# Performance work log

Measured on AMD Instinct MI355X. Metric: run time of the kernel, lower is better.

The kernel has to match this reference:

```python
import jax, jax.numpy as jnp
import numpy as np

B, H, TQ, TK, DH = 4, 8, 128, 128, 64
N_MEM, D_MEM, TOPK, HID = 100000, 512, 32, 128


def setup_inputs() -> dict:
    key = jax.random.key(0)
    ks = jax.random.split(key, 12)
    return {
        "q": jax.random.normal(ks[0], (B, H, TQ, DH), jnp.float32),
        "k_ctx": jax.random.normal(ks[1], (B, H, TK, DH), jnp.float32),
        "v_ctx": jax.random.normal(ks[2], (B, H, TK, DH), jnp.float32),
        "q_for_mem": jax.random.normal(ks[3], (B, TQ, D_MEM), jnp.float32),
        "mem_keys": jax.random.normal(ks[4], (N_MEM, D_MEM), jnp.float32),
        "mem_values": jax.random.normal(ks[5], (N_MEM, D_MEM), jnp.float32),
        "Wk": jax.random.normal(ks[6], (DH, D_MEM), jnp.float32) / np.sqrt(D_MEM),
        "Wv": jax.random.normal(ks[7], (DH, D_MEM), jnp.float32) / np.sqrt(D_MEM),
        "W1": jax.random.normal(ks[8], (HID, 2 * DH), jnp.float32) / np.sqrt(2 * DH),
        "b1": jnp.zeros((HID,), jnp.float32),
        "w2": jax.random.normal(ks[9], (HID,), jnp.float32) / np.sqrt(HID),
        "b2": jnp.zeros((1,), jnp.float32),
    }


def reference(q, k_ctx, v_ctx, q_for_mem, mem_keys, mem_values, Wk, Wv, W1, b1, w2, b2):
    # --- MemoryBank.retrieve: dense scores + top-k gather ---
    mem_scores = jnp.einsum('btd,nd->btn', q_for_mem, mem_keys)          # [B,TQ,N]
    _, idx = jax.lax.top_k(mem_scores, TOPK)                             # [B,TQ,K]
    K_mem = mem_keys[idx] @ Wk.T                                         # [B,TQ,K,DH] (mem_k_proj)
    V_mem = mem_values[idx] @ Wv.T                                       # [B,TQ,K,DH] (mem_v_proj)

    # --- ParametricScoreMLP: f([q;k]) = w2 . relu(W1q q + W1k k + b1) + b2 ---
    W1q, W1k = W1[:, :DH], W1[:, DH:]                                    # split concat linear
    q_part = jnp.einsum('bhtd,ed->bhte', q, W1q)                         # [B,H,TQ,HID]
    kctx_part = jnp.einsum('bhsd,ed->bhse', k_ctx, W1k)                  # [B,H,TK,HID]
    kmem_part = jnp.einsum('btkd,ed->btke', K_mem, W1k)                  # [B,TQ,K,HID]

    h_ctx = jax.nn.relu(q_part[:, :, :, None, :] + kctx_part[:, :, None, :, :] + b1)
    s_ctx = jnp.einsum('bhtse,e->bhts', h_ctx, w2) + b2[0]               # [B,H,TQ,TK]
    h_mem = jax.nn.relu(q_part[:, :, :, None, :] + kmem_part[:, None, :, :, :] + b1)
    s_mem = jnp.einsum('bhtke,e->bhtk', h_mem, w2) + b2[0]               # [B,H,TQ,K]

    scores = jnp.concatenate([s_ctx, s_mem], axis=-1)                    # [B,H,TQ,TK+K]
    weights = jax.nn.softmax(scores, axis=-1)

    w_ctx, w_mem = weights[..., :TK], weights[..., TK:]
    out = jnp.einsum('bhts,bhsd->bhtd', w_ctx, v_ctx) \
        + jnp.einsum('bhtk,btkd->bhtd', w_mem, V_mem)                    # [B,H,TQ,DH]
    return out, weights
```

## Files before the change

kernel.cpp:

```cpp
#include <hip/hip_runtime.h>
#include <cmath>

constexpr int B_ = 4, H_ = 8, TQ_ = 128, TK_ = 128, DH_ = 64;
constexpr int NMEM = 100000, DM = 512, TOPK = 32, HID = 128;
constexpr int R_ = B_ * TQ_;
constexpr int CTILE = 128, RTILE = 64;
constexpr int NCHP = 784;
constexpr int NPAD = NCHP * CTILE;
constexpr int KC = 16;
constexpr int NCAND = NCHP * KC;
constexpr int KSEL = 48;
constexpr int CAP  = 128;
constexpr int NLD  = NCAND / 256;

using f32x4  = __attribute__((ext_vector_type(4))) float;
using bf16x8 = __attribute__((ext_vector_type(8))) short;
using u16x8  = __attribute__((ext_vector_type(8))) unsigned short;

#define GLOAD16(g, l) __builtin_amdgcn_global_load_lds( \
    (const __attribute__((address_space(1))) void*)(g), \
    (__attribute__((address_space(3))) void*)(l), 16, 0, 0)

static __device__ __forceinline__ unsigned short f2bf(float f) {
    unsigned u = __float_as_uint(f);
    u = (u + 0x7FFFu + ((u >> 16) & 1u)) >> 16;
    return (unsigned short)u;
}

__global__ __launch_bounds__(256)
void k0_cvt(const float* __restrict__ src, unsigned short* __restrict__ dst,
            long n, long ntot)
{
    long stride = (long)gridDim.x * 256 * 8;
    for (long base = ((long)blockIdx.x * 256 + threadIdx.x) * 8; base < ntot; base += stride) {
        u16x8 o;
        if (base < n) {
            float4 v0 = *reinterpret_cast<const float4*>(src + base);
            float4 v1 = *reinterpret_cast<const float4*>(src + base + 4);
            o[0] = f2bf(v0.x); o[1] = f2bf(v0.y); o[2] = f2bf(v0.z); o[3] = f2bf(v0.w);
            o[4] = f2bf(v1.x); o[5] = f2bf(v1.y); o[6] = f2bf(v1.z); o[7] = f2bf(v1.w);
        } else {
            o = (u16x8)0;
        }
        *reinterpret_cast<u16x8*>(dst + base) = o;
    }
}

__global__ __launch_bounds__(256)
void k1_mfma(const unsigned short* __restrict__ qmb, const unsigned short* __restrict__ mkb,
             unsigned* __restrict__ cand_k, int* __restrict__ cand_i)
{
    const int wgid = blockIdx.x;
    const int xcd = wgid & 7;
    const int k9 = wgid >> 3;
    const int chunk = xcd * 98 + (k9 >> 3);
    const int rt = k9 & 7;
    const int row0 = rt * RTILE;
    const int col0 = chunk * CTILE;
    const int tid = threadIdx.x;
    const int lane = tid & 63, w = tid >> 6;
    const int wm = w >> 1, wn = w & 1;

    __shared__ __align__(16) char smem[64 * 132 * 4];
    char* Abase = smem;
    char* Bbase = smem + 8192;
    float* scf = (float*)smem;

    const char* srcA[2];
    const char* srcB[4];
#pragma unroll
    for (int p = 0; p < 2; ++p) {
        int X = p * 4096 + w * 1024 + lane * 16;
        int r = X >> 7, c = (X & 127) ^ ((r & 7) << 4);
        srcA[p] = (const char*)qmb + (size_t)(row0 + r) * 1024 + c;
    }
#pragma unroll
    for (int p = 0; p < 4; ++p) {
        int X = p * 4096 + w * 1024 + lane * 16;
        int r = X >> 7, c = (X & 127) ^ ((r & 7) << 4);
        srcB[p] = (const char*)mkb + (size_t)(col0 + r) * 1024 + c;
    }
    int aoff[2][2], boff[4][2];
#pragma unroll
    for (int mi = 0; mi < 2; ++mi) {
        int rr = wm * 32 + mi * 16 + (lane & 15);
        int bse = rr * 128 + ((lane >> 4) * 16);
        aoff[mi][0] = bse ^ ((rr & 7) << 4);
        aoff[mi][1] = (bse + 64) ^ ((rr & 7) << 4);
    }
#pragma unroll
    for (int ni = 0; ni < 4; ++ni) {
        int rr = wn * 64 + ni * 16 + (lane & 15);
        int bse = rr * 128 + ((lane >> 4) * 16);
        boff[ni][0] = 8192 + (bse ^ ((rr & 7) << 4));
        boff[ni][1] = 8192 + ((bse + 64) ^ ((rr & 7) << 4));
    }

    f32x4 acc[2][4];
#pragma unroll
    for (int mi = 0; mi < 2; ++mi)
#pragma unroll
        for (int ni = 0; ni < 4; ++ni) acc[mi][ni] = (f32x4)0.f;

    for (int ks = 0; ks < 8; ++ks) {
#pragma unroll
        for (int p = 0; p < 2; ++p) {
            GLOAD16(srcA[p], Abase + p * 4096 + w * 1024);
            srcA[p] += 128;
        }
#pragma unroll
        for (int p = 0; p < 4; ++p) {
            GLOAD16(srcB[p], Bbase + p * 4096 + w * 1024);
            srcB[p] += 128;
        }
        __syncthreads();
#pragma unroll
        for (int kk = 0; kk < 2; ++kk) {
            bf16x8 af[2], bfr[4];
#pragma unroll
            for (int mi = 0; mi < 2; ++mi)
                af[mi] = *reinterpret_cast<const bf16x8*>(smem + aoff[mi][kk]);
#pragma unroll
            for (int ni = 0; ni < 4; ++ni)
                bfr[ni] = *reinterpret_cast<const bf16x8*>(smem + boff[ni][kk]);
#pragma unroll
            for (int mi = 0; mi < 2; ++mi)
#pragma unroll
                for (int ni = 0; ni < 4; ++ni)
                    acc[mi][ni] = __builtin_amdgcn_mfma_f32_16x16x32_bf16(af[mi], bfr[ni], acc[mi][ni], 0, 0, 0);
        }
        __syncthreads();
    }

#pragma unroll
    for (int mi = 0; mi < 2; ++mi)
#pragma unroll
        for (int ni = 0; ni < 4; ++ni)
#pragma unroll
            for (int reg = 0; reg < 4; ++reg) {
                int rr = wm * 32 + mi * 16 + (lane >> 4) * 4 + reg;
                int cc = wn * 64 + ni * 16 + (lane & 15);
                scf[rr * 132 + cc] = (col0 + cc < NMEM) ? acc[mi][ni][reg] : -INFINITY;
            }
    __syncthreads();

    const int rid = tid >> 2, sub = tid & 3;
    const float* srow = scf + rid * 132;
    unsigned long long t0 = 0ull, t1 = 0ull, t2 = 0ull, t3 = 0ull;
#pragma unroll 8
    for (int i = 0; i < 32; ++i) {
        int c = sub + 4 * i;
        float v = srow[c];
        unsigned b = __float_as_uint(v);
        unsigned s = b ^ ((unsigned)((int)b >> 31) | 0x80000000u);
        unsigned long long k = ((unsigned long long)s << 7) | (unsigned)(127 - c);
        bool g0 = k > t0, g1 = k > t1, g2 = k > t2, g3 = k > t3;
        unsigned long long n0 = g0 ? k : t0;
        unsigned long long n1 = g0 ? t0 : (g1 ? k : t1);
        unsigned long long n2 = g1 ? t1 : (g2 ? k : t2);
        unsigned long long n3 = g2 ? t2 : (g3 ? k : t3);
        t0 = n0; t1 = n1; t2 = n2; t3 = n3;
    }
    size_t base = (size_t)(row0 + rid) * NCAND + (size_t)chunk * KC + sub * 4;
    uint4 kv, iv;
    kv.x = (unsigned)(t0 >> 7); iv.x = col0 + 127 - (int)(t0 & 127u);
    kv.y = (unsigned)(t1 >> 7); iv.y = col0 + 127 - (int)(t1 & 127u);
    kv.z = (unsigned)(t2 >> 7); iv.z = col0 + 127 - (int)(t2 & 127u);
    kv.w = (unsigned)(t3 >> 7); iv.w = col0 + 127 - (int)(t3 & 127u);
    *reinterpret_cast<uint4*>(cand_k + base) = kv;
    *reinterpret_cast<uint4*>(cand_i + base) = iv;
}

__global__ __launch_bounds__(256)
void k2a_thresh(const unsigned* __restrict__ cand_k, const int* __restrict__ cand_i,
                int* __restrict__ cand2_i, int* __restrict__ cand2_n)
{
    const int row = blockIdx.x;
    const int tid = threadIdx.x;
    const int lane = tid & 63, wv = tid >> 6;
    const unsigned* ck = cand_k + (size_t)row * NCAND;

    unsigned key[NLD];
#pragma unroll
    for (int j = 0; j < NLD; ++j) key[j] = ck[tid + j * 256];

    __shared__ int red[4];
    __shared__ int cnt;
    unsigned lo = 0u;
    int c_cur = NCAND;
    for (int bit = 31; bit >= 0; --bit) {
        if (c_cur <= CAP) break;
        unsigned T = lo | (1u << bit);
        int c = 0;
#pragma unroll
        for (int j = 0; j < NLD; ++j) c += (key[j] >= T);
#pragma unroll
        for (int off = 1; off < 64; off <<= 1) c += __shfl_xor(c, off);
        if (lane == 0) red[wv] = c;
        __syncthreads();
        int ct = red[0] + red[1] + red[2] + red[3];
        if (ct >= KSEL) { lo = T; c_cur = ct; }
        __syncthreads();
    }

    if (tid == 0) cnt = 0;
    __syncthreads();
#pragma unroll
    for (int j = 0; j < NLD; ++j) {
        if (key[j] >= lo) {
            int p = atomicAdd(&cnt, 1);
            if (p < CAP) cand2_i[(size_t)row * CAP + p] = cand_i[(size_t)row * NCAND + tid + j * 256];
        }
    }
    __syncthreads();
    if (tid == 0) cand2_n[row] = cnt < CAP ? cnt : CAP;
}

__global__ __launch_bounds__(256)
void k2b_rescore(const float* __restrict__ qm, const float* __restrict__ mk,
                 const int* __restrict__ cand2_i, const int* __restrict__ cand2_n,
                 double* __restrict__ rsc)
{
    const int row = blockIdx.x;
    const int tid = threadIdx.x;
    const int lane = tid & 63, wv = tid >> 6;
    const int c = blockIdx.y * 4 + wv;
    const int n = cand2_n[row];
    if (c >= n) return;
    const int idx = cand2_i[(size_t)row * CAP + c];
    const float* qrow = qm + (size_t)row * DM;
    const float* krow = mk + (size_t)idx * DM;
    double p = 0.0;
#pragma unroll
    for (int j = 0; j < DM / 64; ++j) {
        int d = lane + j * 64;
        p += (double)qrow[d] * (double)krow[d];
    }
#pragma unroll
    for (int off = 1; off < 64; off <<= 1) p += __shfl_xor(p, off);
    if (lane == 0) rsc[(size_t)row * CAP + c] = p;
}

__global__ __launch_bounds__(64)
void k2c_top32(const double* __restrict__ rsc, const int* __restrict__ cand2_i,
               const int* __restrict__ cand2_n, int* __restrict__ sel)
{
    const int row = blockIdx.x;
    const int lane = threadIdx.x;
    const int n = cand2_n[row];
    double v0 = -1.0e300, v1 = -1.0e300;
    int i0 = 0x7fffffff, i1 = 0x7fffffff;
    if (lane < n)      { v0 = rsc[(size_t)row * CAP + lane];      i0 = cand2_i[(size_t)row * CAP + lane]; }
    if (lane + 64 < n) { v1 = rsc[(size_t)row * CAP + lane + 64]; i1 = cand2_i[(size_t)row * CAP + lane + 64]; }
    for (int s = 0; s < TOPK; ++s) {
        double bv; int bi;
        if (v0 > v1 || (v0 == v1 && i0 < i1)) { bv = v0; bi = i0; }
        else                                  { bv = v1; bi = i1; }
#pragma unroll
        for (int off = 1; off < 64; off <<= 1) {
            double ov = __shfl_xor(bv, off);
            int    oi = __shfl_xor(bi, off);
            if (ov > bv || (ov == bv && oi < bi)) { bv = ov; bi = oi; }
        }
        if (lane == 0) sel[row * TOPK + s] = bi;
        if (i0 == bi) v0 = -1.0e300;
        if (i1 == bi) v1 = -1.0e300;
    }
}

__global__ __launch_bounds__(64)
void k3_proj(const float* __restrict__ mk, const float* __restrict__ mv,
             const float* __restrict__ Wk, const float* __restrict__ Wv,
             const int* __restrict__ sel,
             float* __restrict__ Kmem, float* __restrict__ Vmem)
{
    const int i0 = blockIdx.x * 8;
    const int tid = threadIdx.x;
    __shared__ float s[2][8][DM];
    __shared__ int si[8];
    if (tid < 8) si[tid] = sel[i0 + tid];
    __syncthreads();
    for (int l = tid; l < 1024; l += 64) {
        int r = l >> 7, c4 = l & 127;
        *reinterpret_cast<float4*>(&s[0][r][c4 * 4]) =
            *reinterpret_cast<const float4*>(mk + (size_t)si[r] * DM + c4 * 4);
        *reinterpret_cast<float4*>(&s[1][r][c4 * 4]) =
            *reinterpret_cast<const float4*>(mv + (size_t)si[r] * DM + c4 * 4);
    }
    __syncthreads();
    const int doV = tid >> 5;
    const int ep = tid & 31;
    const float* W = doV ? Wv : Wk;
    const float* w0 = W + (size_t)ep * DM;
    const float* w1 = W + (size_t)(ep + 32) * DM;
    float a0[8], a1[8];
#pragma unroll
    for (int r = 0; r < 8; ++r) { a0[r] = 0.f; a1[r] = 0.f; }
    for (int d4 = 0; d4 < DM / 4; ++d4) {
        float4 x0 = *reinterpret_cast<const float4*>(w0 + d4 * 4);
        float4 x1 = *reinterpret_cast<const float4*>(w1 + d4 * 4);
#pragma unroll
        for (int r = 0; r < 8; ++r) {
            float4 m = *reinterpret_cast<const float4*>(&s[doV][r][d4 * 4]);
            a0[r] = fmaf(x0.x, m.x, fmaf(x0.y, m.y, fmaf(x0.z, m.z, fmaf(x0.w, m.w, a0[r]))));
            a1[r] = fmaf(x1.x, m.x, fmaf(x1.y, m.y, fmaf(x1.z, m.z, fmaf(x1.w, m.w, a1[r]))));
        }
    }
    float* O = doV ? Vmem : Kmem;
#pragma unroll
    for (int r = 0; r < 8; ++r) {
        O[(size_t)(i0 + r) * DH_ + ep] = a0[r];
        O[(size_t)(i0 + r) * DH_ + ep + 32] = a1[r];
    }
}

__global__ __launch_bounds__(128)
void k4_parts(const float* __restrict__ q, const float* __restrict__ kctx,
              const float* __restrict__ Kmem, const float* __restrict__ W1,
              float* __restrict__ qp, float* __restrict__ kcp, float* __restrict__ kmp)
{
    const int bid = blockIdx.x;
    const int tid = threadIdx.x;
    const float* src; float* dst; int woff;
    if (bid < 1024)      { int r0 = bid * 4;          src = q    + (size_t)r0 * DH_; dst = qp  + (size_t)r0 * HID; woff = 0; }
    else if (bid < 2048) { int r0 = (bid - 1024) * 4; src = kctx + (size_t)r0 * DH_; dst = kcp + (size_t)r0 * HID; woff = DH_; }
    else                 { int r0 = (bid - 2048) * 4; src = Kmem + (size_t)r0 * DH_; dst = kmp + (size_t)r0 * HID; woff = DH_; }
    __shared__ float s[4][DH_];
    for (int l = tid; l < 4 * DH_; l += 128) s[l >> 6][l & 63] = src[l];
    __syncthreads();
    const float* wr = W1 + (size_t)tid * (2 * DH_) + woff;
    float a0 = 0.f, a1 = 0.f, a2 = 0.f, a3 = 0.f;
#pragma unroll 8
    for (int d = 0; d < DH_; ++d) {
        float w = wr[d];
        a0 = fmaf(s[0][d], w, a0);
        a1 = fmaf(s[1][d], w, a1);
        a2 = fmaf(s[2][d], w, a2);
        a3 = fmaf(s[3][d], w, a3);
    }
    dst[0 * HID + tid] = a0;
    dst[1 * HID + tid] = a1;
    dst[2 * HID + tid] = a2;
    dst[3 * HID + tid] = a3;
}

__global__ __launch_bounds__(256)
void k5_attn(const float* __restrict__ qp, const float* __restrict__ kcp,
             const float* __restrict__ kmp, const float* __restrict__ vctx,
             const float* __restrict__ Vmem, const float* __restrict__ b1,
             const float* __restrict__ w2, const float* __restrict__ b2,
             float* __restrict__ out, float* __restrict__ outw)
{
    const int bid = blockIdx.x;
    const int t = bid & 127, h = (bid >> 7) & 7, b = bid >> 10;
    const int tid = threadIdx.x;
    const int lane = tid & 63, wv = tid >> 6;
    const int bh = b * H_ + h, bht = bh * TQ_ + t, bt = b * TQ_ + t;
    constexpr int NS = TK_ + TOPK;
    __shared__ float qps[HID], b1s[HID], w2s[HID];
    __shared__ float sc[NS];
    __shared__ float red[8];
    if (tid < HID) {
        qps[tid] = qp[(size_t)bht * HID + tid];
        b1s[tid] = b1[tid];
        w2s[tid] = w2[tid];
    }
    __syncthreads();
    const float bias2 = b2[0];
    if (tid < NS) {
        const float* kr = (tid < TK_) ? (kcp + ((size_t)bh * TK_ + tid) * HID)
                                      : (kmp + ((size_t)bt * TOPK + (tid - TK_)) * HID);
        float acc = 0.f;
#pragma unroll 4
        for (int e4 = 0; e4 < HID / 4; ++e4) {
            float4 kv = *reinterpret_cast<const float4*>(kr + e4 * 4);
            acc += fmaxf(qps[e4 * 4 + 0] + kv.x + b1s[e4 * 4 + 0], 0.f) * w2s[e4 * 4 + 0];
            acc += fmaxf(qps[e4 * 4 + 1] + kv.y + b1s[e4 * 4 + 1], 0.f) * w2s[e4 * 4 + 1];
            acc += fmaxf(qps[e4 * 4 + 2] + kv.z + b1s[e4 * 4 + 2], 0.f) * w2s[e4 * 4 + 2];
            acc += fmaxf(qps[e4 * 4 + 3] + kv.w + b1s[e4 * 4 + 3], 0.f) * w2s[e4 * 4 + 3];
        }
        sc[tid] = acc + bias2;
    }
    __syncthreads();
    float v = (tid < NS) ? sc[tid] : -INFINITY;
    float m = v;
#pragma unroll
    for (int off = 1; off < 64; off <<= 1) m = fmaxf(m, __shfl_xor(m, off));
    if (lane == 0) red[wv] = m;
    __syncthreads();
    if (tid == 0) red[4] = fmaxf(fmaxf(red[0], red[1]), fmaxf(red[2], red[3]));
    __syncthreads();
    const float mm = red[4];
    float e = (tid < NS) ? expf(v - mm) : 0.f;
    float ssum = e;
#pragma unroll
    for (int off = 1; off < 64; off <<= 1) ssum += __shfl_xor(ssum, off);
    if (lane == 0) red[wv] = ssum;
    __syncthreads();
    if (tid == 0) red[5] = red[0] + red[1] + red[2] + red[3];
    __syncthreads();
    const float inv = 1.f / red[5];
    if (tid < NS) {
        float w = e * inv;
        sc[tid] = w;
        outw[(size_t)bht * NS + tid] = w;
    }
    __syncthreads();
    if (tid < DH_) {
        float acc = 0.f;
        const float* vb = vctx + (size_t)bh * TK_ * DH_ + tid;
        for (int s2 = 0; s2 < TK_; ++s2) acc = fmaf(sc[s2], vb[(size_t)s2 * DH_], acc);
        const float* vm = Vmem + (size_t)bt * TOPK * DH_ + tid;
#pragma unroll
        for (int kk = 0; kk < TOPK; ++kk) acc = fmaf(sc[TK_ + kk], vm[(size_t)kk * DH_], acc);
        out[(size_t)bht * DH_ + tid] = acc;
    }
}

extern "C" void kernel_launch(void* const* d_in, const int* in_sizes, int n_in,
                              void* d_out, int out_size, void* d_ws, size_t ws_size,
                              hipStream_t stream)
{
    const float* q    = (const float*)d_in[0];
    const float* kctx = (const float*)d_in[1];
    const float* vctx = (const float*)d_in[2];
    const float* qm   = (const float*)d_in[3];
    const float* mk   = (const float*)d_in[4];
    const float* mv   = (const float*)d_in[5];
    const float* Wk   = (const float*)d_in[6];
    const float* Wv   = (const float*)d_in[7];
    const float* W1   = (const float*)d_in[8];
    const float* b1   = (const float*)d_in[9];
    const float* w2   = (const float*)d_in[10];
    const float* b2   = (const float*)d_in[11];
    float* out  = (float*)d_out;
    float* outw = out + (size_t)B_ * H_ * TQ_ * DH_;

    char* w = (char*)d_ws;
    unsigned short* mkb = (unsigned short*)w; w += sizeof(unsigned short) * (size_t)NPAD * DM;
    unsigned short* qmb = (unsigned short*)w; w += sizeof(unsigned short) * R_ * DM;
    unsigned* cand_k = (unsigned*)w; w += sizeof(unsigned) * (size_t)R_ * NCAND;
    int*   cand_i = (int*)w;   w += sizeof(int) * (size_t)R_ * NCAND;
    int*   cand2_i= (int*)w;   w += sizeof(int) * R_ * CAP;
    int*   cand2_n= (int*)w;   w += sizeof(int) * R_;
    double* rsc   = (double*)w; w += sizeof(double) * R_ * CAP;
    int*   sel    = (int*)w;   w += sizeof(int) * R_ * TOPK;
    float* Kmem   = (float*)w; w += sizeof(float) * R_ * TOPK * DH_;
    float* Vmem   = (float*)w; w += sizeof(float) * R_ * TOPK * DH_;
    float* qp     = (float*)w; w += sizeof(float) * B_ * H_ * TQ_ * HID;
    float* kcp    = (float*)w; w += sizeof(float) * B_ * H_ * TK_ * HID;
    float* kmp    = (float*)w; w += sizeof(float) * R_ * TOPK * HID;

    hipLaunchKernelGGL(k0_cvt, dim3(2048), dim3(256), 0, stream,
                       mk, mkb, (long)NMEM * DM, (long)NPAD * DM);
    hipLaunchKernelGGL(k0_cvt, dim3(128), dim3(256), 0, stream,
                       qm, qmb, (long)R_ * DM, (long)R_ * DM);
    hipLaunchKernelGGL(k1_mfma, dim3(NCHP * 8), dim3(256), 0, stream, qmb, mkb, cand_k, cand_i);
    hipLaunchKernelGGL(k2a_thresh, dim3(R_), dim3(256), 0, stream, cand_k, cand_i, cand2_i, cand2_n);
    hipLaunchKernelGGL(k2b_rescore, dim3(R_, CAP / 4), dim3(256), 0, stream, qm, mk, cand2_i, cand2_n, rsc);
    hipLaunchKernelGGL(k2c_top32, dim3(R_), dim3(64), 0, stream, rsc, cand2_i, cand2_n, sel);
    hipLaunchKernelGGL(k3_proj, dim3(R_ * TOPK / 8), dim3(64), 0, stream, mk, mv, Wk, Wv, sel, Kmem, Vmem);
    hipLaunchKernelGGL(k4_parts, dim3(6144), dim3(128), 0, stream, q, kctx, Kmem, W1, qp, kcp, kmp);
    hipLaunchKernelGGL(k5_attn, dim3(B_ * H_ * TQ_), dim3(256), 0, stream, qp, kcp, kmp, vctx, Vmem, b1, w2, b2, out, outw);
}
```

Before: 361.0 us.

## Fuse fp32-to-bf16 conversion into score GEMM with register-staged double buffering

Removes the separate conversion kernels that wrote bf16 copies of the memory keys and queries. The score GEMM now loads fp32 directly into registers, converts by truncation (perm picks the high halves) and writes swizzled bf16 tiles to a double-buffered LDS, prefetching the next k-slice while MFMAs run. This avoids one full read and write pass over the 100k x 512 key matrix, but each GEMM block now reads twice the bytes in fp32, and the 8 row-tile blocks per chunk re-read the same keys. Truncation instead of round-to-nearest also changes the candidate scores slightly.

```diff
diff --git a/kernel.cpp b/kernel.cpp
--- a/kernel.cpp
+++ b/kernel.cpp
@@ -6,7 +6,6 @@
 constexpr int R_ = B_ * TQ_;
 constexpr int CTILE = 128, RTILE = 64;
 constexpr int NCHP = 784;
-constexpr int NPAD = NCHP * CTILE;
 constexpr int KC = 16;
 constexpr int NCAND = NCHP * KC;
 constexpr int KSEL = 48;
@@ -15,39 +14,11 @@
 
 using f32x4  = __attribute__((ext_vector_type(4))) float;
 using bf16x8 = __attribute__((ext_vector_type(8))) short;
-using u16x8  = __attribute__((ext_vector_type(8))) unsigned short;
-
-#define GLOAD16(g, l) __builtin_amdgcn_global_load_lds( \
-    (const __attribute__((address_space(1))) void*)(g), \
-    (__attribute__((address_space(3))) void*)(l), 16, 0, 0)
-
-static __device__ __forceinline__ unsigned short f2bf(float f) {
-    unsigned u = __float_as_uint(f);
-    u = (u + 0x7FFFu + ((u >> 16) & 1u)) >> 16;
-    return (unsigned short)u;
-}
+
+#define PKBF(h, l) (int)__builtin_amdgcn_perm(__float_as_uint(h), __float_as_uint(l), 0x07060302u)
 
 __global__ __launch_bounds__(256)
-void k0_cvt(const float* __restrict__ src, unsigned short* __restrict__ dst,
-            long n, long ntot)
-{
-    long stride = (long)gridDim.x * 256 * 8;
-    for (long base = ((long)blockIdx.x * 256 + threadIdx.x) * 8; base < ntot; base += stride) {
-        u16x8 o;
-        if (base < n) {
-            float4 v0 = *reinterpret_cast<const float4*>(src + base);
-            float4 v1 = *reinterpret_cast<const float4*>(src + base + 4);
-            o[0] = f2bf(v0.x); o[1] = f2bf(v0.y); o[2] = f2bf(v0.z); o[3] = f2bf(v0.w);
-            o[4] = f2bf(v1.x); o[5] = f2bf(v1.y); o[6] = f2bf(v1.z); o[7] = f2bf(v1.w);
-        } else {
-            o = (u16x8)0;
-        }
-        *reinterpret_cast<u16x8*>(dst + base) = o;
-    }
-}
-
-__global__ __launch_bounds__(256)
-void k1_mfma(const unsigned short* __restrict__ qmb, const unsigned short* __restrict__ mkb,
+void k1_mfma(const float* __restrict__ qm, const float* __restrict__ mk,
              unsigned* __restrict__ cand_k, int* __restrict__ cand_i)
 {
     const int wgid = blockIdx.x;
@@ -61,25 +32,9 @@
     const int lane = tid & 63, w = tid >> 6;
     const int wm = w >> 1, wn = w & 1;
 
-    __shared__ __align__(16) char smem[64 * 132 * 4];
-    char* Abase = smem;
-    char* Bbase = smem + 8192;
+    __shared__ __align__(16) char smem[49152];
     float* scf = (float*)smem;
 
-    const char* srcA[2];
-    const char* srcB[4];
-#pragma unroll
-    for (int p = 0; p < 2; ++p) {
-        int X = p * 4096 + w * 1024 + lane * 16;
-        int r = X >> 7, c = (X & 127) ^ ((r & 7) << 4);
-        srcA[p] = (const char*)qmb + (size_t)(row0 + r) * 1024 + c;
-    }
-#pragma unroll
-    for (int p = 0; p < 4; ++p) {
-        int X = p * 4096 + w * 1024 + lane * 16;
-        int r = X >> 7, c = (X & 127) ^ ((r & 7) << 4);
-        srcB[p] = (const char*)mkb + (size_t)(col0 + r) * 1024 + c;
-    }
     int aoff[2][2], boff[4][2];
 #pragma unroll
     for (int mi = 0; mi < 2; ++mi) {
@@ -92,9 +47,49 @@
     for (int ni = 0; ni < 4; ++ni) {
         int rr = wn * 64 + ni * 16 + (lane & 15);
         int bse = rr * 128 + ((lane >> 4) * 16);
-        boff[ni][0] = 8192 + (bse ^ ((rr & 7) << 4));
-        boff[ni][1] = 8192 + ((bse + 64) ^ ((rr & 7) << 4));
-    }
+        boff[ni][0] = bse ^ ((rr & 7) << 4);
+        boff[ni][1] = (bse + 64) ^ ((rr & 7) << 4);
+    }
+
+    const int ar = tid >> 2, ac = (tid & 3) * 16;
+    const int br = tid >> 1, bc = (tid & 1) * 32;
+    const float* aptr = qm + (size_t)(row0 + ar) * DM + ac;
+    const int bgr = col0 + br;
+    const bool bok = bgr < NMEM;
+    const float* bptr = mk + (size_t)(bok ? bgr : 0) * DM + bc;
+    const int aswz = (ar & 7) << 4, cbA = ac * 2;
+    const int bswz = (br & 7) << 4, cbB = bc * 2;
+
+    float4 ra[4], rb[8];
+
+#define LOAD_REGS(KS) do {                                                    \
+    const float* ap_ = aptr + (KS) * 64;                                      \
+    _Pragma("unroll") for (int j = 0; j < 4; ++j)                             \
+        ra[j] = *reinterpret_cast<const float4*>(ap_ + 4 * j);                \
+    const float* bp_ = bptr + (KS) * 64;                                      \
+    _Pragma("unroll") for (int j = 0; j < 8; ++j)                             \
+        rb[j] = *reinterpret_cast<const float4*>(bp_ + 4 * j);                \
+    if (!bok) { _Pragma("unroll") for (int j = 0; j < 8; ++j)                 \
+        rb[j] = make_float4(0.f, 0.f, 0.f, 0.f); }                            \
+} while (0)
+
+#define CVT_STORE(BUF) do {                                                   \
+    char* Ab_ = smem + (BUF) * 8192;                                          \
+    int4 wa0 = make_int4(PKBF(ra[0].y, ra[0].x), PKBF(ra[0].w, ra[0].z),      \
+                         PKBF(ra[1].y, ra[1].x), PKBF(ra[1].w, ra[1].z));     \
+    int4 wa1 = make_int4(PKBF(ra[2].y, ra[2].x), PKBF(ra[2].w, ra[2].z),      \
+                         PKBF(ra[3].y, ra[3].x), PKBF(ra[3].w, ra[3].z));     \
+    *reinterpret_cast<int4*>(Ab_ + ar * 128 + ( cbA       ^ aswz)) = wa0;     \
+    *reinterpret_cast<int4*>(Ab_ + ar * 128 + ((cbA + 16) ^ aswz)) = wa1;     \
+    char* Bb_ = smem + 16384 + (BUF) * 16384;                                 \
+    _Pragma("unroll") for (int j = 0; j < 4; ++j) {                           \
+        int4 wv = make_int4(PKBF(rb[2*j].y,   rb[2*j].x),                     \
+                            PKBF(rb[2*j].w,   rb[2*j].z),                     \
+                            PKBF(rb[2*j+1].y, rb[2*j+1].x),                   \
+                            PKBF(rb[2*j+1].w, rb[2*j+1].z));                  \
+        *reinterpret_cast<int4*>(Bb_ + br * 128 + ((cbB + 16*j) ^ bswz)) = wv;\
+    }                                                                         \
+} while (0)
 
     f32x4 acc[2][4];
 #pragma unroll
@@ -102,34 +97,33 @@
 #pragma unroll
         for (int ni = 0; ni < 4; ++ni) acc[mi][ni] = (f32x4)0.f;
 
+    LOAD_REGS(0);
+    CVT_STORE(0);
+    __syncthreads();
+
+    int cur = 0;
     for (int ks = 0; ks < 8; ++ks) {
-#pragma unroll
-        for (int p = 0; p < 2; ++p) {
-            GLOAD16(srcA[p], Abase + p * 4096 + w * 1024);
-            srcA[p] += 128;
-        }
-#pragma unroll
-        for (int p = 0; p < 4; ++p) {
-            GLOAD16(srcB[p], Bbase + p * 4096 + w * 1024);
-            srcB[p] += 128;
-        }
-        __syncthreads();
+        if (ks < 7) LOAD_REGS(ks + 1);
+        const char* Ab = smem + cur * 8192;
+        const char* Bb = smem + 16384 + cur * 16384;
 #pragma unroll
         for (int kk = 0; kk < 2; ++kk) {
             bf16x8 af[2], bfr[4];
 #pragma unroll
             for (int mi = 0; mi < 2; ++mi)
-                af[mi] = *reinterpret_cast<const bf16x8*>(smem + aoff[mi][kk]);
+                af[mi] = *reinterpret_cast<const bf16x8*>(Ab + aoff[mi][kk]);
 #pragma unroll
             for (int ni = 0; ni < 4; ++ni)
-                bfr[ni] = *reinterpret_cast<const bf16x8*>(smem + boff[ni][kk]);
+                bfr[ni] = *reinterpret_cast<const bf16x8*>(Bb + boff[ni][kk]);
 #pragma unroll
             for (int mi = 0; mi < 2; ++mi)
 #pragma unroll
                 for (int ni = 0; ni < 4; ++ni)
                     acc[mi][ni] = __builtin_amdgcn_mfma_f32_16x16x32_bf16(af[mi], bfr[ni], acc[mi][ni], 0, 0, 0);
         }
+        if (ks < 7) CVT_STORE(cur ^ 1);
         __syncthreads();
+        cur ^= 1;
     }
 
 #pragma unroll
@@ -169,6 +163,8 @@
     kv.w = (unsigned)(t3 >> 7); iv.w = col0 + 127 - (int)(t3 & 127u);
     *reinterpret_cast<uint4*>(cand_k + base) = kv;
     *reinterpret_cast<uint4*>(cand_i + base) = iv;
+#undef LOAD_REGS
+#undef CVT_STORE
 }
 
 __global__ __launch_bounds__(256)
@@ -437,8 +433,6 @@
     float* outw = out + (size_t)B_ * H_ * TQ_ * DH_;
 
     char* w = (char*)d_ws;
-    unsigned short* mkb = (unsigned short*)w; w += sizeof(unsigned short) * (size_t)NPAD * DM;
-    unsigned short* qmb = (unsigned short*)w; w += sizeof(unsigned short) * R_ * DM;
     unsigned* cand_k = (unsigned*)w; w += sizeof(unsigned) * (size_t)R_ * NCAND;
     int*   cand_i = (int*)w;   w += sizeof(int) * (size_t)R_ * NCAND;
     int*   cand2_i= (int*)w;   w += sizeof(int) * R_ * CAP;
@@ -451,11 +445,7 @@
     float* kcp    = (float*)w; w += sizeof(float) * B_ * H_ * TK_ * HID;
     float* kmp    = (float*)w; w += sizeof(float) * R_ * TOPK * HID;
 
-    hipLaunchKernelGGL(k0_cvt, dim3(2048), dim3(256), 0, stream,
-                       mk, mkb, (long)NMEM * DM, (long)NPAD * DM);
-    hipLaunchKernelGGL(k0_cvt, dim3(128), dim3(256), 0, stream,
-                       qm, qmb, (long)R_ * DM, (long)R_ * DM);
-    hipLaunchKernelGGL(k1_mfma, dim3(NCHP * 8), dim3(256), 0, stream, qmb, mkb, cand_k, cand_i);
+    hipLaunchKernelGGL(k1_mfma, dim3(NCHP * 8), dim3(256), 0, stream, qm, mk, cand_k, cand_i);
     hipLaunchKernelGGL(k2a_thresh, dim3(R_), dim3(256), 0, stream, cand_k, cand_i, cand2_i, cand2_n);
     hipLaunchKernelGGL(k2b_rescore, dim3(R_, CAP / 4), dim3(256), 0, stream, qm, mk, cand2_i, cand2_n, rsc);
     hipLaunchKernelGGL(k2c_top32, dim3(R_), dim3(64), 0, stream, rsc, cand2_i, cand2_n, sel);
```

Result: slower. 461.2 us (+27.8%).

## Fold W1k into Wk projection, fuse conversion kernels, vectorize rescore

Applied to the files above, without the earlier changes.

Precomputes a combined matrix W1k·Wk so the memory-key path goes straight from gathered 512-dim keys to 128-dim MLP features in one step, removing the Kmem intermediate and the separate k4 pass over it. The two bf16 conversion launches merge into one, and the rescore kernel now uses float4 loads. The key projection becomes 128x512 instead of 64x512 per row, which adds FLOPs and changes the rounding order. It saves one launch and an intermediate round trip through memory.

```diff
diff --git a/kernel.cpp b/kernel.cpp
--- a/kernel.cpp
+++ b/kernel.cpp
@@ -28,21 +28,47 @@
 }
 
 __global__ __launch_bounds__(256)
-void k0_cvt(const float* __restrict__ src, unsigned short* __restrict__ dst,
-            long n, long ntot)
-{
+void k0_cvt(const float* __restrict__ mk, const float* __restrict__ qm,
+            unsigned short* __restrict__ dst)
+{
+    const long totalmk = (long)NPAD * DM;
+    const long nvalid  = (long)NMEM * DM;
+    const long total   = totalmk + (long)R_ * DM;
     long stride = (long)gridDim.x * 256 * 8;
-    for (long base = ((long)blockIdx.x * 256 + threadIdx.x) * 8; base < ntot; base += stride) {
+    for (long base = ((long)blockIdx.x * 256 + threadIdx.x) * 8; base < total; base += stride) {
         u16x8 o;
-        if (base < n) {
-            float4 v0 = *reinterpret_cast<const float4*>(src + base);
-            float4 v1 = *reinterpret_cast<const float4*>(src + base + 4);
+        const float* src = nullptr;
+        long off = 0;
+        if (base < totalmk) {
+            if (base < nvalid) { src = mk; off = base; }
+        } else { src = qm; off = base - totalmk; }
+        if (src) {
+            float4 v0 = *reinterpret_cast<const float4*>(src + off);
+            float4 v1 = *reinterpret_cast<const float4*>(src + off + 4);
             o[0] = f2bf(v0.x); o[1] = f2bf(v0.y); o[2] = f2bf(v0.z); o[3] = f2bf(v0.w);
             o[4] = f2bf(v1.x); o[5] = f2bf(v1.y); o[6] = f2bf(v1.z); o[7] = f2bf(v1.w);
         } else {
             o = (u16x8)0;
         }
         *reinterpret_cast<u16x8*>(dst + base) = o;
+    }
+}
+
+__global__ __launch_bounds__(256)
+void kW_comb(const float* __restrict__ W1, const float* __restrict__ Wk,
+             float* __restrict__ Wcomb)
+{
+    const int e = blockIdx.x;
+    const int tid = threadIdx.x;
+    __shared__ float w1s[DH_];
+    if (tid < DH_) w1s[tid] = W1[(size_t)e * (2 * DH_) + DH_ + tid];
+    __syncthreads();
+    for (int dm = tid; dm < DM; dm += 256) {
+        float acc = 0.f;
+#pragma unroll 8
+        for (int d = 0; d < DH_; ++d)
+            acc = fmaf(w1s[d], Wk[(size_t)d * DM + dm], acc);
+        Wcomb[(size_t)e * DM + dm] = acc;
     }
 }
 
@@ -228,14 +254,14 @@
     const int n = cand2_n[row];
     if (c >= n) return;
     const int idx = cand2_i[(size_t)row * CAP + c];
-    const float* qrow = qm + (size_t)row * DM;
-    const float* krow = mk + (size_t)idx * DM;
-    double p = 0.0;
-#pragma unroll
-    for (int j = 0; j < DM / 64; ++j) {
-        int d = lane + j * 64;
-        p += (double)qrow[d] * (double)krow[d];
-    }
+    const float4* q4 = reinterpret_cast<const float4*>(qm + (size_t)row * DM);
+    const float4* k4 = reinterpret_cast<const float4*>(mk + (size_t)idx * DM);
+    float4 a0 = q4[lane], b0 = k4[lane];
+    float4 a1 = q4[lane + 64], b1 = k4[lane + 64];
+    double p = (double)a0.x * b0.x + (double)a0.y * b0.y
+             + (double)a0.z * b0.z + (double)a0.w * b0.w
+             + (double)a1.x * b1.x + (double)a1.y * b1.y
+             + (double)a1.z * b1.z + (double)a1.w * b1.w;
 #pragma unroll
     for (int off = 1; off < 64; off <<= 1) p += __shfl_xor(p, off);
     if (lane == 0) rsc[(size_t)row * CAP + c] = p;
@@ -268,63 +294,74 @@
     }
 }
 
-__global__ __launch_bounds__(64)
-void k3_proj(const float* __restrict__ mk, const float* __restrict__ mv,
-             const float* __restrict__ Wk, const float* __restrict__ Wv,
-             const int* __restrict__ sel,
-             float* __restrict__ Kmem, float* __restrict__ Vmem)
-{
-    const int i0 = blockIdx.x * 8;
-    const int tid = threadIdx.x;
-    __shared__ float s[2][8][DM];
-    __shared__ int si[8];
-    if (tid < 8) si[tid] = sel[i0 + tid];
-    __syncthreads();
-    for (int l = tid; l < 1024; l += 64) {
-        int r = l >> 7, c4 = l & 127;
-        *reinterpret_cast<float4*>(&s[0][r][c4 * 4]) =
-            *reinterpret_cast<const float4*>(mk + (size_t)si[r] * DM + c4 * 4);
-        *reinterpret_cast<float4*>(&s[1][r][c4 * 4]) =
-            *reinterpret_cast<const float4*>(mv + (size_t)si[r] * DM + c4 * 4);
-    }
-    __syncthreads();
-    const int doV = tid >> 5;
-    const int ep = tid & 31;
-    const float* W = doV ? Wv : Wk;
-    const float* w0 = W + (size_t)ep * DM;
-    const float* w1 = W + (size_t)(ep + 32) * DM;
-    float a0[8], a1[8];
-#pragma unroll
-    for (int r = 0; r < 8; ++r) { a0[r] = 0.f; a1[r] = 0.f; }
-    for (int d4 = 0; d4 < DM / 4; ++d4) {
-        float4 x0 = *reinterpret_cast<const float4*>(w0 + d4 * 4);
-        float4 x1 = *reinterpret_cast<const float4*>(w1 + d4 * 4);
-#pragma unroll
-        for (int r = 0; r < 8; ++r) {
-            float4 m = *reinterpret_cast<const float4*>(&s[doV][r][d4 * 4]);
-            a0[r] = fmaf(x0.x, m.x, fmaf(x0.y, m.y, fmaf(x0.z, m.z, fmaf(x0.w, m.w, a0[r]))));
-            a1[r] = fmaf(x1.x, m.x, fmaf(x1.y, m.y, fmaf(x1.z, m.z, fmaf(x1.w, m.w, a1[r]))));
-        }
-    }
-    float* O = doV ? Vmem : Kmem;
-#pragma unroll
-    for (int r = 0; r < 8; ++r) {
-        O[(size_t)(i0 + r) * DH_ + ep] = a0[r];
-        O[(size_t)(i0 + r) * DH_ + ep + 32] = a1[r];
+__global__ __launch_bounds__(192)
+void k3_pv(const float* __restrict__ mk, const float* __restrict__ mv,
+           const float* __restrict__ Wv, const float* __restrict__ Wcomb,
+           const int* __restrict__ sel,
+           float* __restrict__ kmp, float* __restrict__ Vmem)
+{
+    const int i0 = blockIdx.x * 16;
+    const int tid = threadIdx.x;
+    __shared__ float sK[16][DM];
+    __shared__ float sV[16][DM];
+    __shared__ int si[16];
+    if (tid < 16) si[tid] = sel[i0 + tid];
+    __syncthreads();
+    for (int l = tid; l < 4096; l += 192) {
+        int mat = l >> 11, r = (l >> 7) & 15, c4 = l & 127;
+        const float* src = (mat ? mv : mk) + (size_t)si[r] * DM + c4 * 4;
+        float4 v = *reinterpret_cast<const float4*>(src);
+        float* dstp = (mat ? &sV[r][c4 * 4] : &sK[r][c4 * 4]);
+        *reinterpret_cast<float4*>(dstp) = v;
+    }
+    __syncthreads();
+
+    if (tid < HID) {
+        const float* wrow = Wcomb + (size_t)tid * DM;
+        float acc[16];
+#pragma unroll
+        for (int r = 0; r < 16; ++r) acc[r] = 0.f;
+        for (int d4 = 0; d4 < DM / 4; ++d4) {
+            float4 wv4 = *reinterpret_cast<const float4*>(wrow + d4 * 4);
+#pragma unroll
+            for (int r = 0; r < 16; ++r) {
+                float4 m = *reinterpret_cast<const float4*>(&sK[r][d4 * 4]);
+                acc[r] = fmaf(wv4.x, m.x, fmaf(wv4.y, m.y, fmaf(wv4.z, m.z, fmaf(wv4.w, m.w, acc[r]))));
+            }
+        }
+#pragma unroll
+        for (int r = 0; r < 16; ++r)
+            kmp[(size_t)(i0 + r) * HID + tid] = acc[r];
+    } else {
+        const int e = tid - HID;
+        const float* wrow = Wv + (size_t)e * DM;
+        float acc[16];
+#pragma unroll
+        for (int r = 0; r < 16; ++r) acc[r] = 0.f;
+        for (int d4 = 0; d4 < DM / 4; ++d4) {
+            float4 wv4 = *reinterpret_cast<const float4*>(wrow + d4 * 4);
+#pragma unroll
+            for (int r = 0; r < 16; ++r) {
+                float4 m = *reinterpret_cast<const float4*>(&sV[r][d4 * 4]);
+                acc[r] = fmaf(wv4.x, m.x, fmaf(wv4.y, m.y, fmaf(wv4.z, m.z, fmaf(wv4.w, m.w, acc[r]))));
+            }
+        }
+#pragma unroll
+        for (int r = 0; r < 16; ++r)
+            Vmem[(size_t)(i0 + r) * DH_ + e] = acc[r];
     }
 }
 
 __global__ __launch_bounds__(128)
 void k4_parts(const float* __restrict__ q, const float* __restrict__ kctx,
-              const float* __restrict__ Kmem, const float* __restrict__ W1,
-              float* __restrict__ qp, float* __restrict__ kcp, float* __restrict__ kmp)
+              const float* __restrict__ W1,
+              float* __restrict__ qp, float* __restrict__ kcp)
 {
     const int bid = blockIdx.x;
     const int tid = threadIdx.x;
     const float* src; float* dst; int woff;
     if (bid < 1024)      { int r0 = bid * 4;          src = q    + (size_t)r0 * DH_; dst = qp  + (size_t)r0 * HID; woff = 0; }
-    else if (bid < 2048) { int r0 = (bid - 1024) * 4; src = kctx + (size_t)r0 * DH_; dst = kcp + (size_t)r0 * HID; woff = DH_; }
-    else                 { int r0 = (bid - 2048) * 4; src = Kmem + (size_t)r0 * DH_; dst = kmp + (size_t)r0 * HID; woff = DH_; }
+    else                 { int r0 = (bid - 1024) * 4; src = kctx + (size_t)r0 * DH_; dst = kcp + (size_t)r0 * HID; woff = DH_; }
     __shared__ float s[4][DH_];
     for (int l = tid; l < 4 * DH_; l += 128) s[l >> 6][l & 63] = src[l];
     __syncthreads();
@@ -439,27 +476,25 @@
     char* w = (char*)d_ws;
     unsigned short* mkb = (unsigned short*)w; w += sizeof(unsigned short) * (size_t)NPAD * DM;
     unsigned short* qmb = (unsigned short*)w; w += sizeof(unsigned short) * R_ * DM;
+    float* Wcomb  = (float*)w; w += sizeof(float) * HID * DM;
     unsigned* cand_k = (unsigned*)w; w += sizeof(unsigned) * (size_t)R_ * NCAND;
     int*   cand_i = (int*)w;   w += sizeof(int) * (size_t)R_ * NCAND;
     int*   cand2_i= (int*)w;   w += sizeof(int) * R_ * CAP;
     int*   cand2_n= (int*)w;   w += sizeof(int) * R_;
     double* rsc   = (double*)w; w += sizeof(double) * R_ * CAP;
     int*   sel    = (int*)w;   w += sizeof(int) * R_ * TOPK;
-    float* Kmem   = (float*)w; w += sizeof(float) * R_ * TOPK * DH_;
     float* Vmem   = (float*)w; w += sizeof(float) * R_ * TOPK * DH_;
     float* qp     = (float*)w; w += sizeof(float) * B_ * H_ * TQ_ * HID;
     float* kcp    = (float*)w; w += sizeof(float) * B_ * H_ * TK_ * HID;
     float* kmp    = (float*)w; w += sizeof(float) * R_ * TOPK * HID;
 
-    hipLaunchKernelGGL(k0_cvt, dim3(2048), dim3(256), 0, stream,
-                       mk, mkb, (long)NMEM * DM, (long)NPAD * DM);
-    hipLaunchKernelGGL(k0_cvt, dim3(128), dim3(256), 0, stream,
-                       qm, qmb, (long)R_ * DM, (long)R_ * DM);
+    hipLaunchKernelGGL(k0_cvt, dim3(4096), dim3(256), 0, stream, mk, qm, mkb);
+    hipLaunchKernelGGL(kW_comb, dim3(HID), dim3(256), 0, stream, W1, Wk, Wcomb);
     hipLaunchKernelGGL(k1_mfma, dim3(NCHP * 8), dim3(256), 0, stream, qmb, mkb, cand_k, cand_i);
     hipLaunchKernelGGL(k2a_thresh, dim3(R_), dim3(256), 0, stream, cand_k, cand_i, cand2_i, cand2_n);
     hipLaunchKernelGGL(k2b_rescore, dim3(R_, CAP / 4), dim3(256), 0, stream, qm, mk, cand2_i, cand2_n, rsc);
     hipLaunchKernelGGL(k2c_top32, dim3(R_), dim3(64), 0, stream, rsc, cand2_i, cand2_n, sel);
-    hipLaunchKernelGGL(k3_proj, dim3(R_ * TOPK / 8), dim3(64), 0, stream, mk, mv, Wk, Wv, sel, Kmem, Vmem);
-    hipLaunchKernelGGL(k4_parts, dim3(6144), dim3(128), 0, stream, q, kctx, Kmem, W1, qp, kcp, kmp);
+    hipLaunchKernelGGL(k3_pv, dim3(R_ * TOPK / 16), dim3(192), 0, stream, mk, mv, Wv, Wcomb, sel, kmp, Vmem);
+    hipLaunchKernelGGL(k4_parts, dim3(2048), dim3(128), 0, stream, q, kctx, W1, qp, kcp);
     hipLaunchKernelGGL(k5_attn, dim3(B_ * H_ * TQ_), dim3(256), 0, stream, qp, kcp, kmp, vctx, Vmem, b1, w2, b2, out, outw);
 }
```

Result: slower. 384.2 us (+6.4%).

## Enlarge score GEMM row tile to 128, merge conversion kernels, vectorize rescore

Applied to the files above, without the earlier changes.

The memory-score MFMA kernel now covers 128 query rows per workgroup instead of 64. Each memory-key tile is loaded once for twice as many rows, which halves the grid and the global traffic for keys. Because LDS can only hold half the score tile, the per-chunk top-4 extraction runs in two passes. The two bf16 conversion launches are merged into one kernel that writes keys and queries into the adjacent workspace, which relies on qmb directly following mkb. The fp64 rescore now uses float4 loads. The costs are higher register pressure from the 4x4 accumulators and extra barriers.

```diff
diff --git a/kernel.cpp b/kernel.cpp
--- a/kernel.cpp
+++ b/kernel.cpp
@@ -4,7 +4,7 @@
 constexpr int B_ = 4, H_ = 8, TQ_ = 128, TK_ = 128, DH_ = 64;
 constexpr int NMEM = 100000, DM = 512, TOPK = 32, HID = 128;
 constexpr int R_ = B_ * TQ_;
-constexpr int CTILE = 128, RTILE = 64;
+constexpr int CTILE = 128, RTILE = 128;
 constexpr int NCHP = 784;
 constexpr int NPAD = NCHP * CTILE;
 constexpr int KC = 16;
@@ -28,15 +28,23 @@
 }
 
 __global__ __launch_bounds__(256)
-void k0_cvt(const float* __restrict__ src, unsigned short* __restrict__ dst,
-            long n, long ntot)
-{
+void k0_cvt(const float* __restrict__ mk, const float* __restrict__ qm,
+            unsigned short* __restrict__ dst)
+{
+    const long totalmk = (long)NPAD * DM;
+    const long nvalid  = (long)NMEM * DM;
+    const long total   = totalmk + (long)R_ * DM;
     long stride = (long)gridDim.x * 256 * 8;
-    for (long base = ((long)blockIdx.x * 256 + threadIdx.x) * 8; base < ntot; base += stride) {
+    for (long base = ((long)blockIdx.x * 256 + threadIdx.x) * 8; base < total; base += stride) {
         u16x8 o;
-        if (base < n) {
-            float4 v0 = *reinterpret_cast<const float4*>(src + base);
-            float4 v1 = *reinterpret_cast<const float4*>(src + base + 4);
+        const float* src = nullptr;
+        long off = 0;
+        if (base < totalmk) {
+            if (base < nvalid) { src = mk; off = base; }
+        } else { src = qm; off = base - totalmk; }
+        if (src) {
+            float4 v0 = *reinterpret_cast<const float4*>(src + off);
+            float4 v1 = *reinterpret_cast<const float4*>(src + off + 4);
             o[0] = f2bf(v0.x); o[1] = f2bf(v0.y); o[2] = f2bf(v0.z); o[3] = f2bf(v0.w);
             o[4] = f2bf(v1.x); o[5] = f2bf(v1.y); o[6] = f2bf(v1.z); o[7] = f2bf(v1.w);
         } else {
@@ -53,8 +61,8 @@
     const int wgid = blockIdx.x;
     const int xcd = wgid & 7;
     const int k9 = wgid >> 3;
-    const int chunk = xcd * 98 + (k9 >> 3);
-    const int rt = k9 & 7;
+    const int chunk = xcd * 98 + (k9 >> 2);
+    const int rt = k9 & 3;
     const int row0 = rt * RTILE;
     const int col0 = chunk * CTILE;
     const int tid = threadIdx.x;
@@ -63,27 +71,22 @@
 
     __shared__ __align__(16) char smem[64 * 132 * 4];
     char* Abase = smem;
-    char* Bbase = smem + 8192;
+    char* Bbase = smem + 16384;
     float* scf = (float*)smem;
 
-    const char* srcA[2];
+    const char* srcA[4];
     const char* srcB[4];
 #pragma unroll
-    for (int p = 0; p < 2; ++p) {
+    for (int p = 0; p < 4; ++p) {
         int X = p * 4096 + w * 1024 + lane * 16;
         int r = X >> 7, c = (X & 127) ^ ((r & 7) << 4);
         srcA[p] = (const char*)qmb + (size_t)(row0 + r) * 1024 + c;
-    }
-#pragma unroll
-    for (int p = 0; p < 4; ++p) {
-        int X = p * 4096 + w * 1024 + lane * 16;
-        int r = X >> 7, c = (X & 127) ^ ((r & 7) << 4);
         srcB[p] = (const char*)mkb + (size_t)(col0 + r) * 1024 + c;
     }
-    int aoff[2][2], boff[4][2];
-#pragma unroll
-    for (int mi = 0; mi < 2; ++mi) {
-        int rr = wm * 32 + mi * 16 + (lane & 15);
+    int aoff[4][2], boff[4][2];
+#pragma unroll
+    for (int mi = 0; mi < 4; ++mi) {
+        int rr = wm * 64 + mi * 16 + (lane & 15);
         int bse = rr * 128 + ((lane >> 4) * 16);
         aoff[mi][0] = bse ^ ((rr & 7) << 4);
         aoff[mi][1] = (bse + 64) ^ ((rr & 7) << 4);
@@ -92,39 +95,36 @@
     for (int ni = 0; ni < 4; ++ni) {
         int rr = wn * 64 + ni * 16 + (lane & 15);
         int bse = rr * 128 + ((lane >> 4) * 16);
-        boff[ni][0] = 8192 + (bse ^ ((rr & 7) << 4));
-        boff[ni][1] = 8192 + ((bse + 64) ^ ((rr & 7) << 4));
-    }
-
-    f32x4 acc[2][4];
-#pragma unroll
-    for (int mi = 0; mi < 2; ++mi)
+        boff[ni][0] = 16384 + (bse ^ ((rr & 7) << 4));
+        boff[ni][1] = 16384 + ((bse + 64) ^ ((rr & 7) << 4));
+    }
+
+    f32x4 acc[4][4];
+#pragma unroll
+    for (int mi = 0; mi < 4; ++mi)
 #pragma unroll
         for (int ni = 0; ni < 4; ++ni) acc[mi][ni] = (f32x4)0.f;
 
     for (int ks = 0; ks < 8; ++ks) {
 #pragma unroll
-        for (int p = 0; p < 2; ++p) {
+        for (int p = 0; p < 4; ++p) {
             GLOAD16(srcA[p], Abase + p * 4096 + w * 1024);
             srcA[p] += 128;
-        }
-#pragma unroll
-        for (int p = 0; p < 4; ++p) {
             GLOAD16(srcB[p], Bbase + p * 4096 + w * 1024);
             srcB[p] += 128;
         }
         __syncthreads();
 #pragma unroll
         for (int kk = 0; kk < 2; ++kk) {
-            bf16x8 af[2], bfr[4];
-#pragma unroll
-            for (int mi = 0; mi < 2; ++mi)
+            bf16x8 af[4], bfr[4];
+#pragma unroll
+            for (int mi = 0; mi < 4; ++mi)
                 af[mi] = *reinterpret_cast<const bf16x8*>(smem + aoff[mi][kk]);
 #pragma unroll
             for (int ni = 0; ni < 4; ++ni)
                 bfr[ni] = *reinterpret_cast<const bf16x8*>(smem + boff[ni][kk]);
 #pragma unroll
-            for (int mi = 0; mi < 2; ++mi)
+            for (int mi = 0; mi < 4; ++mi)
 #pragma unroll
                 for (int ni = 0; ni < 4; ++ni)
                     acc[mi][ni] = __builtin_amdgcn_mfma_f32_16x16x32_bf16(af[mi], bfr[ni], acc[mi][ni], 0, 0, 0);
@@ -132,43 +132,49 @@
         __syncthreads();
     }
 
-#pragma unroll
-    for (int mi = 0; mi < 2; ++mi)
-#pragma unroll
-        for (int ni = 0; ni < 4; ++ni)
-#pragma unroll
-            for (int reg = 0; reg < 4; ++reg) {
-                int rr = wm * 32 + mi * 16 + (lane >> 4) * 4 + reg;
-                int cc = wn * 64 + ni * 16 + (lane & 15);
-                scf[rr * 132 + cc] = (col0 + cc < NMEM) ? acc[mi][ni][reg] : -INFINITY;
-            }
-    __syncthreads();
-
     const int rid = tid >> 2, sub = tid & 3;
-    const float* srow = scf + rid * 132;
-    unsigned long long t0 = 0ull, t1 = 0ull, t2 = 0ull, t3 = 0ull;
+#pragma unroll
+    for (int h = 0; h < 2; ++h) {
+        if (wm == h) {
+#pragma unroll
+            for (int mi = 0; mi < 4; ++mi)
+#pragma unroll
+                for (int ni = 0; ni < 4; ++ni)
+#pragma unroll
+                    for (int reg = 0; reg < 4; ++reg) {
+                        int rr = mi * 16 + (lane >> 4) * 4 + reg;
+                        int cc = wn * 64 + ni * 16 + (lane & 15);
+                        scf[rr * 132 + cc] = (col0 + cc < NMEM) ? acc[mi][ni][reg] : -INFINITY;
+                    }
+        }
+        __syncthreads();
+
+        const float* srow = scf + rid * 132;
+        unsigned long long t0 = 0ull, t1 = 0ull, t2 = 0ull, t3 = 0ull;
 #pragma unroll 8
-    for (int i = 0; i < 32; ++i) {
-        int c = sub + 4 * i;
-        float v = srow[c];
-        unsigned b = __float_as_uint(v);
-        unsigned s = b ^ ((unsigned)((int)b >> 31) | 0x80000000u);
-        unsigned long long k = ((unsigned long long)s << 7) | (unsigned)(127 - c);
-        bool g0 = k > t0, g1 = k > t1, g2 = k > t2, g3 = k > t3;
-        unsigned long long n0 = g0 ? k : t0;
-        unsigned long long n1 = g0 ? t0 : (g1 ? k : t1);
-        unsigned long long n2 = g1 ? t1 : (g2 ? k : t2);
-        unsigned long long n3 = g2 ? t2 : (g3 ? k : t3);
-        t0 = n0; t1 = n1; t2 = n2; t3 = n3;
-    }
-    size_t base = (size_t)(row0 + rid) * NCAND + (size_t)chunk * KC + sub * 4;
-    uint4 kv, iv;
-    kv.x = (unsigned)(t0 >> 7); iv.x = col0 + 127 - (int)(t0 & 127u);
-    kv.y = (unsigned)(t1 >> 7); iv.y = col0 + 127 - (int)(t1 & 127u);
-    kv.z = (unsigned)(t2 >> 7); iv.z = col0 + 127 - (int)(t2 & 127u);
-    kv.w = (unsigned)(t3 >> 7); iv.w = col0 + 127 - (int)(t3 & 127u);
-    *reinterpret_cast<uint4*>(cand_k + base) = kv;
-    *reinterpret_cast<uint4*>(cand_i + base) = iv;
+        for (int i = 0; i < 32; ++i) {
+            int c = sub + 4 * i;
+            float v = srow[c];
+            unsigned b = __float_as_uint(v);
+            unsigned s = b ^ ((unsigned)((int)b >> 31) | 0x80000000u);
+            unsigned long long k = ((unsigned long long)s << 7) | (unsigned)(127 - c);
+            bool g0 = k > t0, g1 = k > t1, g2 = k > t2, g3 = k > t3;
+            unsigned long long n0 = g0 ? k : t0;
+            unsigned long long n1 = g0 ? t0 : (g1 ? k : t1);
+            unsigned long long n2 = g1 ? t1 : (g2 ? k : t2);
+            unsigned long long n3 = g2 ? t2 : (g3 ? k : t3);
+            t0 = n0; t1 = n1; t2 = n2; t3 = n3;
+        }
+        size_t base = (size_t)(row0 + h * 64 + rid) * NCAND + (size_t)chunk * KC + sub * 4;
+        uint4 kv, iv;
+        kv.x = (unsigned)(t0 >> 7); iv.x = col0 + 127 - (int)(t0 & 127u);
+        kv.y = (unsigned)(t1 >> 7); iv.y = col0 + 127 - (int)(t1 & 127u);
+        kv.z = (unsigned)(t2 >> 7); iv.z = col0 + 127 - (int)(t2 & 127u);
+        kv.w = (unsigned)(t3 >> 7); iv.w = col0 + 127 - (int)(t3 & 127u);
+        *reinterpret_cast<uint4*>(cand_k + base) = kv;
+        *reinterpret_cast<uint4*>(cand_i + base) = iv;
+        __syncthreads();
+    }
 }
 
 __global__ __launch_bounds__(256)
@@ -228,14 +234,14 @@
     const int n = cand2_n[row];
     if (c >= n) return;
     const int idx = cand2_i[(size_t)row * CAP + c];
-    const float* qrow = qm + (size_t)row * DM;
-    const float* krow = mk + (size_t)idx * DM;
-    double p = 0.0;
-#pragma unroll
-    for (int j = 0; j < DM / 64; ++j) {
-        int d = lane + j * 64;
-        p += (double)qrow[d] * (double)krow[d];
-    }
+    const float4* q4 = reinterpret_cast<const float4*>(qm + (size_t)row * DM);
+    const float4* k4 = reinterpret_cast<const float4*>(mk + (size_t)idx * DM);
+    float4 a0 = q4[lane], b0 = k4[lane];
+    float4 a1 = q4[lane + 64], b1 = k4[lane + 64];
+    double p = (double)a0.x * b0.x + (double)a0.y * b0.y
+             + (double)a0.z * b0.z + (double)a0.w * b0.w
+             + (double)a1.x * b1.x + (double)a1.y * b1.y
+             + (double)a1.z * b1.z + (double)a1.w * b1.w;
 #pragma unroll
     for (int off = 1; off < 64; off <<= 1) p += __shfl_xor(p, off);
     if (lane == 0) rsc[(size_t)row * CAP + c] = p;
@@ -451,11 +457,8 @@
     float* kcp    = (float*)w; w += sizeof(float) * B_ * H_ * TK_ * HID;
     float* kmp    = (float*)w; w += sizeof(float) * R_ * TOPK * HID;
 
-    hipLaunchKernelGGL(k0_cvt, dim3(2048), dim3(256), 0, stream,
-                       mk, mkb, (long)NMEM * DM, (long)NPAD * DM);
-    hipLaunchKernelGGL(k0_cvt, dim3(128), dim3(256), 0, stream,
-                       qm, qmb, (long)R_ * DM, (long)R_ * DM);
-    hipLaunchKernelGGL(k1_mfma, dim3(NCHP * 8), dim3(256), 0, stream, qmb, mkb, cand_k, cand_i);
+    hipLaunchKernelGGL(k0_cvt, dim3(4096), dim3(256), 0, stream, mk, qm, mkb);
+    hipLaunchKernelGGL(k1_mfma, dim3(NCHP * 4), dim3(256), 0, stream, qmb, mkb, cand_k, cand_i);
     hipLaunchKernelGGL(k2a_thresh, dim3(R_), dim3(256), 0, stream, cand_k, cand_i, cand2_i, cand2_n);
     hipLaunchKernelGGL(k2b_rescore, dim3(R_, CAP / 4), dim3(256), 0, stream, qm, mk, cand2_i, cand2_n, rsc);
     hipLaunchKernelGGL(k2c_top32, dim3(R_), dim3(64), 0, stream, rsc, cand2_i, cand2_n, sel);
```

Result: slower. 379.9 us (+5.2%).
